# Kernel tuning notes

Measured on AMD Instinct MI355X. Metric: run time of the kernel, lower is better.

Reference implementation:

```python
import jax, jax.numpy as jnp
import numpy as np

NUM_ITEMS = 1_000_000
D = 100           # d_model, args.d
NHEAD = 4
FF = 2048         # TransformerEncoderLayer default dim_feedforward
EPS = 1e-5


def layer_norm(x, g, b):
    m = x.mean(-1, keepdims=True)
    v = ((x - m) ** 2).mean(-1, keepdims=True)
    return (x - m) / jnp.sqrt(v + EPS) * g + b


def setup_inputs() -> dict:
    key = jax.random.key(0)
    ks = jax.random.split(key, 16)
    B, L, K = 16384, 50, 100
    inp = {
        "item_seq": jax.random.randint(ks[0], (B, L), 0, NUM_ITEMS, dtype=jnp.int32),
        "items_to_predict": jax.random.randint(ks[1], (B, K), 0, 100, dtype=jnp.int32),
        # embeddings (init: normal(0, 1/dim)), rec_b zeroed as in source
        "item_emb_w": jax.random.normal(ks[2], (NUM_ITEMS, D), jnp.float32) * (1.0 / D),
        "rec_emb_w": jax.random.normal(ks[3], (100, D), jnp.float32) * (1.0 / D),
        "rec_b_w": jnp.zeros((NUM_ITEMS, 1), jnp.float32),
        # TransformerEncoderLayer params
        "in_proj_w": jax.random.normal(ks[4], (3 * D, D), jnp.float32) * 0.05,
        "in_proj_b": jnp.zeros((3 * D,), jnp.float32),
        "out_proj_w": jax.random.normal(ks[5], (D, D), jnp.float32) * 0.05,
        "out_proj_b": jnp.zeros((D,), jnp.float32),
        "ln1_g": jnp.ones((D,), jnp.float32),
        "ln1_b": jnp.zeros((D,), jnp.float32),
        "ln2_g": jnp.ones((D,), jnp.float32),
        "ln2_b": jnp.zeros((D,), jnp.float32),
        "ffn_w1": jax.random.normal(ks[6], (FF, D), jnp.float32) * 0.05,
        "ffn_b1": jnp.zeros((FF,), jnp.float32),
        "ffn_w2": jax.random.normal(ks[7], (D, FF), jnp.float32) * 0.05,
        "ffn_b2": jnp.zeros((D,), jnp.float32),
    }
    return inp


def reference(item_seq, items_to_predict, item_emb_w, rec_emb_w, rec_b_w,
              in_proj_w, in_proj_b, out_proj_w, out_proj_b,
              ln1_g, ln1_b, ln2_g, ln2_b,
              ffn_w1, ffn_b1, ffn_w2, ffn_b2):
    # Fused gather + segment-sum: replaces the per-sequence Python loop.
    x = item_emb_w[item_seq].sum(axis=1)            # [B, D]

    # TransformerEncoderLayer (norm_first=False, relu, eval/no-dropout).
    # Input is [seq_len=1, batch=B, D]; self-attention over a single position:
    # softmax of one score is exactly 1, so attn output = out_proj(v).
    qkv = x @ in_proj_w.T + in_proj_b               # [B, 3D]
    v = qkv[:, 2 * D:]                              # value projection [B, D]
    attn_out = v @ out_proj_w.T + out_proj_b
    x = layer_norm(x + attn_out, ln1_g, ln1_b)
    ff = jax.nn.relu(x @ ffn_w1.T + ffn_b1) @ ffn_w2.T + ffn_b2
    seq_embs = layer_norm(x + ff, ln2_g, ln2_b)     # [B, D]

    rec = rec_emb_w[items_to_predict]               # [B, K, D]
    b = rec_b_w[items_to_predict][..., 0]           # [B, K]
    # baddbmm(b, rec, seq_embs.unsqueeze(2)).squeeze() -> [B, K]
    res = b + jnp.einsum('bkd,bd->bk', rec, seq_embs)
    return res
```

## Files before the change

kernel.cpp:

```cpp
#include <hip/hip_runtime.h>

#define NB   16384
#define LSEQ 50
#define D    100
#define KP   100
#define FF   2048
#define CH   128
#define NCH  (FF/CH)
#define ROWS 32
#define EPSV 1e-5f
#define SWB  136

typedef unsigned short u16;
typedef unsigned int   u32;
typedef __attribute__((ext_vector_type(8))) short bf16x8;
typedef __attribute__((ext_vector_type(4))) float f32x4;

#define WVP_OFF  0
#define WOP_OFF  14336
#define W1P_OFF  28672
#define W2P_OFF  290816
#define REC_OFF  520192
#define PREP_N   530192

__device__ __forceinline__ float bflo(u32 u){ return __uint_as_float(u << 16); }
__device__ __forceinline__ float bfhi(u32 u){ return __uint_as_float(u & 0xffff0000u); }
__device__ __forceinline__ u16 f2bf(float f){
    u32 b = __float_as_uint(f);
    b += 0x7fffu + ((b >> 16) & 1u);
    return (u16)(b >> 16);
}

__global__ __launch_bounds__(256) void k_prep(
    const float* __restrict__ ipw, const float* __restrict__ opw,
    const float* __restrict__ w1,  const float* __restrict__ w2,
    const float* __restrict__ rec, u16* __restrict__ dst)
{
    int i = blockIdx.x * 256 + threadIdx.x;
    if (i >= PREP_N) return;
    if (i < WOP_OFF) {
        int n = i >> 7, k = i & 127;
        dst[i] = (n < D && k < D) ? f2bf(ipw[2*D*D + n*D + k]) : (u16)0;
    } else if (i < W1P_OFF) {
        int j = i - WOP_OFF; int n = j >> 7, k = j & 127;
        dst[i] = (n < D && k < D) ? f2bf(opw[n*D + k]) : (u16)0;
    } else if (i < W2P_OFF) {
        int j = i - W1P_OFF; int n = j >> 7, k = j & 127;
        dst[i] = (k < D) ? f2bf(w1[n*D + k]) : (u16)0;
    } else if (i < REC_OFF) {
        int j = i - W2P_OFF; int c = j >> 11, jj = j & 2047;
        dst[i] = (c < D) ? f2bf(w2[c*FF + jj]) : (u16)0;
    } else {
        int j = i - REC_OFF;
        dst[i] = f2bf(rec[j]);
    }
}

__global__ __launch_bounds__(256) void k_gather(const int* __restrict__ seq,
        const float* __restrict__ emb, float* __restrict__ xout)
{
    __shared__ float2 part[5][50];
    const int row = blockIdx.x;
    const int t   = threadIdx.x;
    const int c2  = t % 50;
    const int lg  = t / 50;
    float ax = 0.f, ay = 0.f;
    if (lg < 5) {
        const float2* e2 = (const float2*)emb;
        #pragma unroll
        for (int u = 0; u < 10; ++u) {
            int idx = seq[row * LSEQ + lg * 10 + u];
            float2 w = e2[(size_t)idx * 50 + c2];
            ax += w.x; ay += w.y;
        }
        float2 p; p.x = ax; p.y = ay;
        part[lg][c2] = p;
    }
    __syncthreads();
    if (t < 50) {
        float sx = 0.f, sy = 0.f;
        #pragma unroll
        for (int g = 0; g < 5; ++g) { sx += part[g][t].x; sy += part[g][t].y; }
        float2 v; v.x = sx; v.y = sy;
        ((float2*)xout)[(size_t)row * 50 + t] = v;
    }
}

__device__ __forceinline__ void gemm2x2(
    const u16* __restrict__ Alds, const u16* __restrict__ Blds,
    int n0, int nvalid, int fl, int fq, f32x4 acc[2][2])
{
    #pragma unroll
    for (int ks = 0; ks < 4; ++ks) {
        const int kb = ks * 32 + fq * 8;
        bf16x8 a0 = *(const bf16x8*)(Alds + fl * SWB + kb);
        bf16x8 a1 = *(const bf16x8*)(Alds + (16 + fl) * SWB + kb);
        bf16x8 b0 = *(const bf16x8*)(Blds + (n0 + fl) * SWB + kb);
        acc[0][0] = __builtin_amdgcn_mfma_f32_16x16x32_bf16(a0, b0, acc[0][0], 0, 0, 0);
        acc[1][0] = __builtin_amdgcn_mfma_f32_16x16x32_bf16(a1, b0, acc[1][0], 0, 0, 0);
        if (nvalid > 1) {
            bf16x8 b1 = *(const bf16x8*)(Blds + (n0 + 16 + fl) * SWB + kb);
            acc[0][1] = __builtin_amdgcn_mfma_f32_16x16x32_bf16(a0, b1, acc[0][1], 0, 0, 0);
            acc[1][1] = __builtin_amdgcn_mfma_f32_16x16x32_bf16(a1, b1, acc[1][1], 0, 0, 0);
        }
    }
}

template<bool TOBF>
__device__ __forceinline__ void ln_tile(float* __restrict__ A, u16* __restrict__ dstbf,
        const float* __restrict__ g, const float* __restrict__ b, int tid)
{
    const int r  = tid >> 3;
    const int s8 = tid & 7;
    float sum = 0.f, sq = 0.f;
    for (int k = s8; k < D; k += 8) {
        float v = A[r * 104 + k];
        sum += v; sq += v * v;
    }
    sum += __shfl_xor(sum, 1, 64); sq += __shfl_xor(sq, 1, 64);
    sum += __shfl_xor(sum, 2, 64); sq += __shfl_xor(sq, 2, 64);
    sum += __shfl_xor(sum, 4, 64); sq += __shfl_xor(sq, 4, 64);
    float m   = sum * 0.01f;
    float var = sq * 0.01f - m * m;
    float rs  = rsqrtf(var + EPSV);
    for (int k = s8; k < D; k += 8) {
        float v = A[r * 104 + k];
        float y = (v - m) * rs * g[k] + b[k];
        A[r * 104 + k] = y;
        if (TOBF) dstbf[r * SWB + k] = f2bf(y);
    }
}

__global__ __launch_bounds__(256) void k_fused(
    const float* __restrict__ xin,
    const int*  __restrict__ ipred,
    const u16*  __restrict__ wbase,
    const float* __restrict__ rec_b,
    const float* __restrict__ in_proj_b, const float* __restrict__ out_proj_b,
    const float* __restrict__ ln1g, const float* __restrict__ ln1b,
    const float* __restrict__ ln2g, const float* __restrict__ ln2b,
    const float* __restrict__ b1, const float* __restrict__ b2,
    float* __restrict__ out)
{
    __shared__ __align__(16) float A0[ROWS * 104];
    __shared__ __align__(16) u16   Abf[ROWS * SWB];
    __shared__ __align__(16) u16   Hbf[ROWS * SWB];
    __shared__ __align__(16) u16   Wbuf[128 * SWB];

    const int tid  = threadIdx.x;
    const int wv   = tid >> 6;
    const int lane = tid & 63;
    const int fl   = lane & 15;
    const int fq   = lane >> 4;
    const int row0 = blockIdx.x * ROWS;
    const int n0   = wv * 32;
    const int nv7  = (wv < 3) ? 2 : 1;

    const u16* Wvp = wbase + WVP_OFF;
    const u16* Wop = wbase + WOP_OFF;
    const u16* W1p = wbase + W1P_OFF;
    const u16* W2p = wbase + W2P_OFF;
    const u16* recp= wbase + REC_OFF;

    for (int i = tid; i < ROWS * 128; i += 256) {
        int r = i >> 7, k = i & 127;
        float v = (k < D) ? xin[(size_t)(row0 + r) * D + k] : 0.f;
        if (k < D) A0[r * 104 + k] = v;
        Abf[r * SWB + k] = f2bf(v);
    }
    for (int i = tid; i < 112 * 16; i += 256) {
        int r = i >> 4, cb = (i & 15) * 8;
        *(uint4*)(Wbuf + r * SWB + cb) = *(const uint4*)(Wvp + r * 128 + cb);
    }
    __syncthreads();

    {
        f32x4 acc[2][2] = {};
        gemm2x2(Abf, Wbuf, n0, nv7, fl, fq, acc);
        __syncthreads();
        for (int t = 0; t < nv7; ++t) {
            int c = n0 + t * 16 + fl;
            if (c < D) {
                float bvc = in_proj_b[2 * D + c];
                #pragma unroll
                for (int r = 0; r < 4; ++r) {
                    int m = fq * 4 + r;
                    Abf[m * SWB + c]        = f2bf(acc[0][t][r] + bvc);
                    Abf[(16 + m) * SWB + c] = f2bf(acc[1][t][r] + bvc);
                }
            }
        }
        for (int i = tid; i < 112 * 16; i += 256) {
            int r = i >> 4, cb = (i & 15) * 8;
            *(uint4*)(Wbuf + r * SWB + cb) = *(const uint4*)(Wop + r * 128 + cb);
        }
        __syncthreads();
    }

    {
        f32x4 acc[2][2] = {};
        gemm2x2(Abf, Wbuf, n0, nv7, fl, fq, acc);
        for (int t = 0; t < nv7; ++t) {
            int c = n0 + t * 16 + fl;
            if (c < D) {
                float boc = out_proj_b[c];
                #pragma unroll
                for (int r = 0; r < 4; ++r) {
                    int m = fq * 4 + r;
                    A0[m * 104 + c]        += acc[0][t][r] + boc;
                    A0[(16 + m) * 104 + c] += acc[1][t][r] + boc;
                }
            }
        }
        __syncthreads();
    }

    ln_tile<true>(A0, Abf, ln1g, ln1b, tid);

    f32x4 facc[2][2] = {};
    for (int ch = 0; ch < NCH; ++ch) {
        __syncthreads();
        {
            const u16* src = W1p + (size_t)ch * CH * 128;
            for (int i = tid; i < 128 * 16; i += 256) {
                int r = i >> 4, cb = (i & 15) * 8;
                *(uint4*)(Wbuf + r * SWB + cb) = *(const uint4*)(src + r * 128 + cb);
            }
        }
        __syncthreads();
        f32x4 hacc[2][2] = {};
        gemm2x2(Abf, Wbuf, n0, 2, fl, fq, hacc);
        __syncthreads();
        #pragma unroll
        for (int t = 0; t < 2; ++t) {
            int c = n0 + t * 16 + fl;
            float b1c = b1[ch * CH + c];
            #pragma unroll
            for (int r = 0; r < 4; ++r) {
                int m = fq * 4 + r;
                Hbf[m * SWB + c]        = f2bf(fmaxf(hacc[0][t][r] + b1c, 0.f));
                Hbf[(16 + m) * SWB + c] = f2bf(fmaxf(hacc[1][t][r] + b1c, 0.f));
            }
        }
        {
            const u16* src = W2p + ch * CH;
            for (int i = tid; i < 112 * 16; i += 256) {
                int r = i >> 4, cb = (i & 15) * 8;
                *(uint4*)(Wbuf + r * SWB + cb) = *(const uint4*)(src + (size_t)r * FF + cb);
            }
        }
        __syncthreads();
        gemm2x2(Hbf, Wbuf, n0, nv7, fl, fq, facc);
    }

    for (int t = 0; t < nv7; ++t) {
        int c = n0 + t * 16 + fl;
        if (c < D) {
            float b2c = b2[c];
            #pragma unroll
            for (int r = 0; r < 4; ++r) {
                int m = fq * 4 + r;
                A0[m * 104 + c]        += facc[0][t][r] + b2c;
                A0[(16 + m) * 104 + c] += facc[1][t][r] + b2c;
            }
        }
    }
    __syncthreads();

    ln_tile<false>(A0, nullptr, ln2g, ln2b, tid);
    for (int i = tid; i < 1250; i += 256)
        *(uint4*)(Wbuf + i * 8) = *(const uint4*)(recp + i * 8);
    __syncthreads();

    for (int o = tid; o < ROWS * KP; o += 256) {
        int r = o / KP, k = o % KP;
        int grow = row0 + r;
        int idx  = ipred[(size_t)grow * KP + k];
        float s  = rec_b[idx];
        const float* sr = &A0[r * 104];
        const u16*   rr = Wbuf + idx * D;
        for (int d = 0; d < D; d += 2) {
            u32 rv = *(const u32*)(rr + d);
            s += sr[d] * bflo(rv) + sr[d + 1] * bfhi(rv);
        }
        out[(size_t)grow * KP + k] = s;
    }
}

extern "C" void kernel_launch(void* const* d_in, const int* in_sizes, int n_in,
                              void* d_out, int out_size, void* d_ws, size_t ws_size,
                              hipStream_t stream)
{
    const int*   item_seq   = (const int*)d_in[0];
    const int*   ipred      = (const int*)d_in[1];
    const float* item_emb   = (const float*)d_in[2];
    const float* rec_emb    = (const float*)d_in[3];
    const float* rec_b      = (const float*)d_in[4];
    const float* in_proj_w  = (const float*)d_in[5];
    const float* in_proj_b  = (const float*)d_in[6];
    const float* out_proj_w = (const float*)d_in[7];
    const float* out_proj_b = (const float*)d_in[8];
    const float* ln1g = (const float*)d_in[9];
    const float* ln1b = (const float*)d_in[10];
    const float* ln2g = (const float*)d_in[11];
    const float* ln2b = (const float*)d_in[12];
    const float* w1   = (const float*)d_in[13];
    const float* b1   = (const float*)d_in[14];
    const float* w2   = (const float*)d_in[15];
    const float* b2   = (const float*)d_in[16];

    float* xws   = (float*)d_ws;
    u16*   wbase = (u16*)((float*)d_ws + (size_t)NB * D);

    k_prep<<<(PREP_N + 255) / 256, 256, 0, stream>>>(
        in_proj_w, out_proj_w, w1, w2, rec_emb, wbase);
    k_gather<<<NB, 256, 0, stream>>>(item_seq, item_emb, xws);
    k_fused<<<NB / ROWS, 256, 0, stream>>>(xws, ipred, wbase, rec_b,
        in_proj_b, out_proj_b, ln1g, ln1b, ln2g, ln2b, b1, b2, (float*)d_out);
}
```

Baseline: 680.7 us.

## Fold value/out projections, prefetch W1 in registers, score via MFMA GEMM

The value projection and out_proj are pre-multiplied in the prep kernel into one 100x100 matrix with a combined bias, removing one per-block GEMM and its weight reload. W1 chunks are prefetched into registers during the previous chunk's GEMM, and W2 loads are issued earlier, to overlap global loads with MFMA work. The final scoring, previously a scalar dot-product loop per (row, item), becomes one MFMA GEMM of the normalized embeddings against all 100 rec rows, followed by a gather per predicted index. Costs are extra register pressure, a slightly different bf16 rounding of the folded weights, and dependence on the rec table having only 100 rows.

```diff
diff --git a/kernel.cpp b/kernel.cpp
--- a/kernel.cpp
+++ b/kernel.cpp
@@ -16,12 +16,11 @@
 typedef __attribute__((ext_vector_type(8))) short bf16x8;
 typedef __attribute__((ext_vector_type(4))) float f32x4;
 
-#define WVP_OFF  0
-#define WOP_OFF  14336
-#define W1P_OFF  28672
-#define W2P_OFF  290816
-#define REC_OFF  520192
-#define PREP_N   530192
+#define WCP_OFF  0
+#define W1P_OFF  14336
+#define W2P_OFF  276480
+#define RECP_OFF 505856
+#define PREP_N   520192
 
 __device__ __forceinline__ float bflo(u32 u){ return __uint_as_float(u << 16); }
 __device__ __forceinline__ float bfhi(u32 u){ return __uint_as_float(u & 0xffff0000u); }
@@ -33,26 +32,39 @@
 
 __global__ __launch_bounds__(256) void k_prep(
     const float* __restrict__ ipw, const float* __restrict__ opw,
+    const float* __restrict__ ipb, const float* __restrict__ opb,
     const float* __restrict__ w1,  const float* __restrict__ w2,
-    const float* __restrict__ rec, u16* __restrict__ dst)
+    const float* __restrict__ rec, u16* __restrict__ dst,
+    float* __restrict__ bcomb)
 {
     int i = blockIdx.x * 256 + threadIdx.x;
-    if (i >= PREP_N) return;
-    if (i < WOP_OFF) {
+    if (i >= PREP_N + 128) return;
+    if (i < W1P_OFF) {
         int n = i >> 7, k = i & 127;
-        dst[i] = (n < D && k < D) ? f2bf(ipw[2*D*D + n*D + k]) : (u16)0;
-    } else if (i < W1P_OFF) {
-        int j = i - WOP_OFF; int n = j >> 7, k = j & 127;
-        dst[i] = (n < D && k < D) ? f2bf(opw[n*D + k]) : (u16)0;
+        float a = 0.f;
+        if (n < D && k < D) {
+            for (int j = 0; j < D; ++j)
+                a += opw[n * D + j] * ipw[(2 * D + j) * D + k];
+        }
+        dst[i] = f2bf(a);
     } else if (i < W2P_OFF) {
-        int j = i - W1P_OFF; int n = j >> 7, k = j & 127;
-        dst[i] = (k < D) ? f2bf(w1[n*D + k]) : (u16)0;
-    } else if (i < REC_OFF) {
+        int j = i - W1P_OFF; int r = j >> 7, k = j & 127;
+        dst[i] = (k < D) ? f2bf(w1[r * D + k]) : (u16)0;
+    } else if (i < RECP_OFF) {
         int j = i - W2P_OFF; int c = j >> 11, jj = j & 2047;
-        dst[i] = (c < D) ? f2bf(w2[c*FF + jj]) : (u16)0;
+        dst[i] = (c < D) ? f2bf(w2[c * FF + jj]) : (u16)0;
+    } else if (i < PREP_N) {
+        int j = i - RECP_OFF; int n = j >> 7, k = j & 127;
+        dst[i] = (n < D && k < D) ? f2bf(rec[n * D + k]) : (u16)0;
     } else {
-        int j = i - REC_OFF;
-        dst[i] = f2bf(rec[j]);
+        int n = i - PREP_N;
+        float a = 0.f;
+        if (n < D) {
+            a = opb[n];
+            for (int j = 0; j < D; ++j)
+                a += opw[n * D + j] * ipb[2 * D + j];
+        }
+        bcomb[n] = a;
     }
 }
 
@@ -136,7 +148,7 @@
     const int*  __restrict__ ipred,
     const u16*  __restrict__ wbase,
     const float* __restrict__ rec_b,
-    const float* __restrict__ in_proj_b, const float* __restrict__ out_proj_b,
+    const float* __restrict__ bcomb,
     const float* __restrict__ ln1g, const float* __restrict__ ln1b,
     const float* __restrict__ ln2g, const float* __restrict__ ln2b,
     const float* __restrict__ b1, const float* __restrict__ b2,
@@ -146,6 +158,7 @@
     __shared__ __align__(16) u16   Abf[ROWS * SWB];
     __shared__ __align__(16) u16   Hbf[ROWS * SWB];
     __shared__ __align__(16) u16   Wbuf[128 * SWB];
+    __shared__ float sRB[112];
 
     const int tid  = threadIdx.x;
     const int wv   = tid >> 6;
@@ -156,11 +169,10 @@
     const int n0   = wv * 32;
     const int nv7  = (wv < 3) ? 2 : 1;
 
-    const u16* Wvp = wbase + WVP_OFF;
-    const u16* Wop = wbase + WOP_OFF;
+    const u16* Wcp = wbase + WCP_OFF;
     const u16* W1p = wbase + W1P_OFF;
     const u16* W2p = wbase + W2P_OFF;
-    const u16* recp= wbase + REC_OFF;
+    const u16* recp= wbase + RECP_OFF;
 
     for (int i = tid; i < ROWS * 128; i += 256) {
         int r = i >> 7, k = i & 127;
@@ -170,32 +182,10 @@
     }
     for (int i = tid; i < 112 * 16; i += 256) {
         int r = i >> 4, cb = (i & 15) * 8;
-        *(uint4*)(Wbuf + r * SWB + cb) = *(const uint4*)(Wvp + r * 128 + cb);
-    }
+        *(uint4*)(Wbuf + r * SWB + cb) = *(const uint4*)(Wcp + r * 128 + cb);
+    }
+    if (tid < D) sRB[tid] = rec_b[tid];
     __syncthreads();
-
-    {
-        f32x4 acc[2][2] = {};
-        gemm2x2(Abf, Wbuf, n0, nv7, fl, fq, acc);
-        __syncthreads();
-        for (int t = 0; t < nv7; ++t) {
-            int c = n0 + t * 16 + fl;
-            if (c < D) {
-                float bvc = in_proj_b[2 * D + c];
-                #pragma unroll
-                for (int r = 0; r < 4; ++r) {
-                    int m = fq * 4 + r;
-                    Abf[m * SWB + c]        = f2bf(acc[0][t][r] + bvc);
-                    Abf[(16 + m) * SWB + c] = f2bf(acc[1][t][r] + bvc);
-                }
-            }
-        }
-        for (int i = tid; i < 112 * 16; i += 256) {
-            int r = i >> 4, cb = (i & 15) * 8;
-            *(uint4*)(Wbuf + r * SWB + cb) = *(const uint4*)(Wop + r * 128 + cb);
-        }
-        __syncthreads();
-    }
 
     {
         f32x4 acc[2][2] = {};
@@ -203,12 +193,12 @@
         for (int t = 0; t < nv7; ++t) {
             int c = n0 + t * 16 + fl;
             if (c < D) {
-                float boc = out_proj_b[c];
+                float bc = bcomb[c];
                 #pragma unroll
                 for (int r = 0; r < 4; ++r) {
                     int m = fq * 4 + r;
-                    A0[m * 104 + c]        += acc[0][t][r] + boc;
-                    A0[(16 + m) * 104 + c] += acc[1][t][r] + boc;
+                    A0[m * 104 + c]        += acc[0][t][r] + bc;
+                    A0[(16 + m) * 104 + c] += acc[1][t][r] + bc;
                 }
             }
         }
@@ -217,20 +207,47 @@
 
     ln_tile<true>(A0, Abf, ln1g, ln1b, tid);
 
+    uint4 w1r[8], w2r[7];
+    #pragma unroll
+    for (int j = 0; j < 8; ++j) {
+        int idx = j * 256 + tid;
+        int r = idx >> 4, cb = (idx & 15) * 8;
+        w1r[j] = *(const uint4*)(W1p + r * 128 + cb);
+    }
     f32x4 facc[2][2] = {};
     for (int ch = 0; ch < NCH; ++ch) {
         __syncthreads();
-        {
-            const u16* src = W1p + (size_t)ch * CH * 128;
-            for (int i = tid; i < 128 * 16; i += 256) {
-                int r = i >> 4, cb = (i & 15) * 8;
-                *(uint4*)(Wbuf + r * SWB + cb) = *(const uint4*)(src + r * 128 + cb);
-            }
+        #pragma unroll
+        for (int j = 0; j < 8; ++j) {
+            int idx = j * 256 + tid;
+            int r = idx >> 4, cb = (idx & 15) * 8;
+            *(uint4*)(Wbuf + r * SWB + cb) = w1r[j];
+        }
+        #pragma unroll
+        for (int j = 0; j < 7; ++j) {
+            int idx = j * 256 + tid;
+            int r = idx >> 4, cb = (idx & 15) * 8;
+            w2r[j] = *(const uint4*)(W2p + ch * CH + (size_t)r * FF + cb);
         }
         __syncthreads();
         f32x4 hacc[2][2] = {};
         gemm2x2(Abf, Wbuf, n0, 2, fl, fq, hacc);
-        __syncthreads();
+        if (ch < NCH - 1) {
+            const u16* src = W1p + (size_t)(ch + 1) * CH * 128;
+            #pragma unroll
+            for (int j = 0; j < 8; ++j) {
+                int idx = j * 256 + tid;
+                int r = idx >> 4, cb = (idx & 15) * 8;
+                w1r[j] = *(const uint4*)(src + r * 128 + cb);
+            }
+        }
+        __syncthreads();
+        #pragma unroll
+        for (int j = 0; j < 7; ++j) {
+            int idx = j * 256 + tid;
+            int r = idx >> 4, cb = (idx & 15) * 8;
+            *(uint4*)(Wbuf + r * SWB + cb) = w2r[j];
+        }
         #pragma unroll
         for (int t = 0; t < 2; ++t) {
             int c = n0 + t * 16 + fl;
@@ -240,13 +257,6 @@
                 int m = fq * 4 + r;
                 Hbf[m * SWB + c]        = f2bf(fmaxf(hacc[0][t][r] + b1c, 0.f));
                 Hbf[(16 + m) * SWB + c] = f2bf(fmaxf(hacc[1][t][r] + b1c, 0.f));
-            }
-        }
-        {
-            const u16* src = W2p + ch * CH;
-            for (int i = tid; i < 112 * 16; i += 256) {
-                int r = i >> 4, cb = (i & 15) * 8;
-                *(uint4*)(Wbuf + r * SWB + cb) = *(const uint4*)(src + (size_t)r * FF + cb);
             }
         }
         __syncthreads();
@@ -267,23 +277,35 @@
     }
     __syncthreads();
 
-    ln_tile<false>(A0, nullptr, ln2g, ln2b, tid);
-    for (int i = tid; i < 1250; i += 256)
-        *(uint4*)(Wbuf + i * 8) = *(const uint4*)(recp + i * 8);
+    ln_tile<true>(A0, Abf, ln2g, ln2b, tid);
+    for (int i = tid; i < 112 * 16; i += 256) {
+        int r = i >> 4, cb = (i & 15) * 8;
+        *(uint4*)(Wbuf + r * SWB + cb) = *(const uint4*)(recp + r * 128 + cb);
+    }
     __syncthreads();
 
+    {
+        f32x4 acc[2][2] = {};
+        gemm2x2(Abf, Wbuf, n0, nv7, fl, fq, acc);
+        for (int t = 0; t < nv7; ++t) {
+            int c = n0 + t * 16 + fl;
+            if (c < D) {
+                #pragma unroll
+                for (int r = 0; r < 4; ++r) {
+                    int m = fq * 4 + r;
+                    A0[m * 104 + c]        = acc[0][t][r];
+                    A0[(16 + m) * 104 + c] = acc[1][t][r];
+                }
+            }
+        }
+        __syncthreads();
+    }
+
     for (int o = tid; o < ROWS * KP; o += 256) {
-        int r = o / KP, k = o % KP;
+        int r = o / KP, k = o - r * KP;
         int grow = row0 + r;
         int idx  = ipred[(size_t)grow * KP + k];
-        float s  = rec_b[idx];
-        const float* sr = &A0[r * 104];
-        const u16*   rr = Wbuf + idx * D;
-        for (int d = 0; d < D; d += 2) {
-            u32 rv = *(const u32*)(rr + d);
-            s += sr[d] * bflo(rv) + sr[d + 1] * bfhi(rv);
-        }
-        out[(size_t)grow * KP + k] = s;
+        out[(size_t)grow * KP + k] = sRB[idx] + A0[r * 104 + idx];
     }
 }
 
@@ -309,12 +331,13 @@
     const float* w2   = (const float*)d_in[15];
     const float* b2   = (const float*)d_in[16];
 
-    float* xws   = (float*)d_ws;
-    u16*   wbase = (u16*)((float*)d_ws + (size_t)NB * D);
-
-    k_prep<<<(PREP_N + 255) / 256, 256, 0, stream>>>(
-        in_proj_w, out_proj_w, w1, w2, rec_emb, wbase);
+    float* xws    = (float*)d_ws;
+    float* bcombf = xws + (size_t)NB * D;
+    u16*   wbase  = (u16*)(bcombf + 128);
+
+    k_prep<<<(PREP_N + 128 + 255) / 256, 256, 0, stream>>>(
+        in_proj_w, out_proj_w, in_proj_b, out_proj_b, w1, w2, rec_emb, wbase, bcombf);
     k_gather<<<NB, 256, 0, stream>>>(item_seq, item_emb, xws);
-    k_fused<<<NB / ROWS, 256, 0, stream>>>(xws, ipred, wbase, rec_b,
-        in_proj_b, out_proj_b, ln1g, ln1b, ln2g, ln2b, b1, b2, (float*)d_out);
-}
+    k_fused<<<NB / ROWS, 256, 0, stream>>>(xws, ipred, wbase, rec_b, bcombf,
+        ln1g, ln1b, ln2g, ln2b, b1, b2, (float*)d_out);
+}
```

New measurement: 740.2 us. 8.7% more time.
